# Kernel tuning notes

Measured on AMD Instinct MI355X. Metric: run time of the kernel, lower is better.

## Reference

```python
import jax, jax.numpy as jnp
import numpy as np

B, S, D = 2, 2048, 1024
H, DA, DL = 8, 64, 64   # heads, attention_dim, linear_dim
L = 2                    # num_blocks


def _layernorm(x, w, b, eps):
    mu = jnp.mean(x, axis=-1, keepdims=True)
    var = jnp.mean(jnp.square(x - mu), axis=-1, keepdims=True)
    return (x - mu) * jax.lax.rsqrt(var + eps) * w + b


def _norm_no_affine(x, eps):
    mu = jnp.mean(x, axis=-1, keepdims=True)
    var = jnp.mean(jnp.square(x - mu), axis=-1, keepdims=True)
    return (x - mu) * jax.lax.rsqrt(var + eps)


def setup_inputs() -> dict:
    key = jax.random.key(0)
    ks = jax.random.split(key, 8)
    x = jax.random.normal(ks[0], (B, S, D), dtype=jnp.float32)
    # causal visibility mask: True = visible
    attn_mask = jnp.tril(jnp.ones((S, S), dtype=bool))[None].repeat(B, axis=0)
    proj_dim = DL * 2 * H + DA * 2 * H  # 2048
    uvqk = jax.random.normal(ks[1], (L, D, proj_dim), dtype=jnp.float32) * 0.02
    o_w = jax.random.normal(ks[2], (L, D, DL * H), dtype=jnp.float32) * 0.02  # torch [out,in]
    o_b = jnp.zeros((L, D), dtype=jnp.float32)
    ln_w = jnp.ones((L, D), dtype=jnp.float32)
    ln_b = jnp.zeros((L, D), dtype=jnp.float32)
    last_ln_w = jnp.ones((D,), dtype=jnp.float32)
    last_ln_b = jnp.zeros((D,), dtype=jnp.float32)
    return {"x": x, "attn_mask": attn_mask, "uvqk": uvqk, "o_w": o_w,
            "o_b": o_b, "ln_w": ln_w, "ln_b": ln_b,
            "last_ln_w": last_ln_w, "last_ln_b": last_ln_b}


def reference(x, attn_mask, uvqk, o_w, o_b, ln_w, ln_b, last_ln_w, last_ln_b):
    seq_len = x.shape[1]
    m = attn_mask[:, None, :, :]  # [B,1,S,S]
    for i in range(L):
        h = _layernorm(x, ln_w[i], ln_b[i], 1e-6)                 # [B,S,D]
        proj = jax.nn.silu(jnp.einsum('bsd,de->bse', h, uvqk[i]))  # [B,S,2*(DL+DA)*H]
        u, v, q, k = jnp.split(proj, [DL * H, 2 * DL * H, 2 * DL * H + DA * H], axis=-1)
        q = q.reshape(B, seq_len, H, DA).transpose(0, 2, 1, 3)   # [B,H,S,DA]
        kk = k.reshape(B, seq_len, H, DA).transpose(0, 2, 1, 3)
        vv = v.reshape(B, seq_len, H, DL).transpose(0, 2, 1, 3)  # [B,H,S,DL]
        uu = u.reshape(B, seq_len, H, DL).transpose(0, 2, 1, 3)
        scores = jnp.einsum('bhsd,bhtd->bhst', q, kk)            # [B,H,S,S]
        scores = jnp.where(m, jax.nn.silu(scores) / seq_len, 0.0)
        out = jnp.einsum('bhst,bhtd->bhsd', scores, vv)          # [B,H,S,DL]
        out = _norm_no_affine(out, 1e-6)
        u_dot = (uu * out).transpose(0, 2, 1, 3).reshape(B, seq_len, DL * H)
        x = x + jnp.einsum('bsf,df->bsd', u_dot, o_w[i]) + o_b[i]
    return _layernorm(x, last_ln_w, last_ln_b, 1e-8)
```

## Files before the change

### kernel.cpp

```cpp
#include <hip/hip_runtime.h>

#define B_ 2
#define S_ 2048
#define D_ 1024
#define H_ 8
#define L_ 2
#define P_ 2048
#define F_ 512
#define R_ (B_*S_)

typedef unsigned short u16;
typedef unsigned int u32;
typedef __bf16 bf16;
typedef bf16 bf16x8 __attribute__((ext_vector_type(8)));
typedef short short8 __attribute__((ext_vector_type(8)));
typedef float v4f __attribute__((ext_vector_type(4)));

__device__ __forceinline__ float silu_fast(float x){
  float e = __expf(-x);
  return x * __builtin_amdgcn_rcpf(1.0f + e);
}
__device__ __forceinline__ float bf2f(u16 u){
  union { u32 i; float f; } x; x.i = ((u32)u) << 16; return x.f;
}
__device__ __forceinline__ u16 f2bfu(float f){
  union { float f; u32 i; } x; x.f = f;
  u32 r = x.i + 0x7fff + ((x.i >> 16) & 1);
  return (u16)(r >> 16);
}
__device__ __forceinline__ u16 f2bft(float f){
  union { float f; u32 i; } x; x.f = f;
  return (u16)(x.i >> 16);
}
__device__ __forceinline__ void gload16(const u16* g, u16* l){
  __builtin_amdgcn_global_load_lds(
      (const __attribute__((address_space(1))) void*)g,
      (__attribute__((address_space(3))) void*)l, 16, 0, 0);
}

__global__ __launch_bounds__(256) void cvt_bf16_kernel(const float* __restrict__ src, u16* __restrict__ dst){
  int i = (blockIdx.x * 256 + threadIdx.x) * 4;
  float4 v = *(const float4*)(src + i);
  ushort4 o; o.x = f2bfu(v.x); o.y = f2bfu(v.y); o.z = f2bfu(v.z); o.w = f2bfu(v.w);
  *(ushort4*)(dst + i) = o;
}

__global__ __launch_bounds__(256) void cvt_uvqkT_kernel(const float* __restrict__ uvqk, u16* __restrict__ ot){
  __shared__ float t[32][33];
  int l = blockIdx.z;
  int p0 = blockIdx.x * 32, d0 = blockIdx.y * 32;
  int tx = threadIdx.x & 31, ty = threadIdx.x >> 5;
  const float* src = uvqk + ((size_t)l * D_ + d0) * P_ + p0;
  #pragma unroll
  for (int s = 0; s < 4; s++)
    t[ty + s*8][tx] = src[(size_t)(ty + s*8) * P_ + tx];
  __syncthreads();
  u16* dst = ot + ((size_t)l * P_ + p0) * D_ + d0;
  #pragma unroll
  for (int s = 0; s < 4; s++)
    dst[(size_t)(ty + s*8) * D_ + tx] = f2bfu(t[tx][ty + s*8]);
}

__global__ __launch_bounds__(256) void kvpack_kernel(const u16* __restrict__ projh,
    u16* __restrict__ kpack, u16* __restrict__ vpack){
  __shared__ u16 tls[64*72];
  int t = blockIdx.x, t0 = t * 64;
  int bh = blockIdx.y;
  int b = bh >> 3, hh = bh & 7;
  int tid = threadIdx.x;
  const size_t bS = (size_t)b * S_;
  const int voff = F_ + hh*64, koff = 3*F_ + hh*64;
  {
    int row = tid >> 2, c16 = (tid & 3) * 16;
    const u16* sp = projh + (bS + t0 + row) * P_ + voff + c16;
    short8 a = *(const short8*)sp;
    short8 bq = *(const short8*)(sp + 8);
    *(short8*)&tls[row*72 + c16] = a;
    *(short8*)&tls[row*72 + c16 + 8] = bq;
  }
  __syncthreads();
  size_t obase = ((size_t)(bh*32 + t) * 8) * 512;
  #pragma unroll
  for (int pass = 0; pass < 2; pass++){
    int id = tid + pass * 256;
    int c = id >> 6, lane = id & 63;
    int quad = lane >> 4, l15 = lane & 15;
    int cns = c >> 1, ckst = c & 1;
    const u16* kp = projh + (bS + t0 + cns*16 + l15) * P_ + koff + ckst*32 + quad*8;
    *(short8*)(kpack + obase + (size_t)c*512 + lane*8) = *(const short8*)kp;
    short8 vv;
    #pragma unroll
    for (int j = 0; j < 8; j++)
      vv[j] = (short)tls[(ckst*32 + quad*8 + j)*72 + cns*16 + l15];
    *(short8*)(vpack + obase + (size_t)c*512 + lane*8) = vv;
  }
}

__global__ __launch_bounds__(256) void ln_kernel(const float* __restrict__ src,
    const float* __restrict__ w, const float* __restrict__ b,
    void* __restrict__ outp, float eps, int out_bf16){
  int row = blockIdx.x, tid = threadIdx.x;
  const float* xr = src + (size_t)row * D_;
  float4 v = *(const float4*)(xr + tid * 4);
  float s  = v.x + v.y + v.z + v.w;
  float sq = v.x*v.x + v.y*v.y + v.z*v.z + v.w*v.w;
  #pragma unroll
  for (int off = 32; off; off >>= 1){ s += __shfl_down(s, off); sq += __shfl_down(sq, off); }
  __shared__ float red[8];
  __shared__ float stats[2];
  int wid = tid >> 6;
  if ((tid & 63) == 0){ red[wid] = s; red[4 + wid] = sq; }
  __syncthreads();
  if (tid == 0){
    float S1 = red[0] + red[1] + red[2] + red[3];
    float S2 = red[4] + red[5] + red[6] + red[7];
    float mu = S1 * (1.0f / D_);
    float var = S2 * (1.0f / D_) - mu * mu;
    stats[0] = mu; stats[1] = rsqrtf(var + eps);
  }
  __syncthreads();
  float mu = stats[0], rs = stats[1];
  int i = tid * 4;
  float4 wv = *(const float4*)(w + i);
  float4 bv = *(const float4*)(b + i);
  float o0 = (v.x - mu) * rs * wv.x + bv.x;
  float o1 = (v.y - mu) * rs * wv.y + bv.y;
  float o2 = (v.z - mu) * rs * wv.z + bv.z;
  float o3 = (v.w - mu) * rs * wv.w + bv.w;
  if (out_bf16){
    ushort4 o; o.x = f2bfu(o0); o.y = f2bfu(o1); o.z = f2bfu(o2); o.w = f2bfu(o3);
    *(ushort4*)((u16*)outp + (size_t)row * D_ + i) = o;
  } else {
    *(float4*)((float*)outp + (size_t)row * D_ + i) = make_float4(o0, o1, o2, o3);
  }
}

template<int KDIM, int BKC>
__device__ __forceinline__ void gemm_mfma_core(const u16* __restrict__ A,
    const u16* __restrict__ Bt, u16* As, u16* Bs, int m0, int n0, v4f acc[4][4]){
  int tid = threadIdx.x;
  int w = tid >> 6, lane = tid & 63;
  int wm = w >> 1, wn = w & 1, quad = lane >> 4, l15 = lane & 15;
  int srow = lane >> 2, skoct = (lane & 3) * 8;
  for (int kt = 0; kt < KDIM; kt += BKC*32){
    __syncthreads();
    #pragma unroll
    for (int s = 0; s < 2; s++){
      int g = w * 2 + s;
      #pragma unroll
      for (int kc = 0; kc < BKC; kc++){
        gload16(A  + (size_t)(m0 + g*16 + srow) * KDIM + kt + kc*32 + skoct,
                As + (g*BKC + kc)*512);
        gload16(Bt + (size_t)(n0 + g*16 + srow) * KDIM + kt + kc*32 + skoct,
                Bs + (g*BKC + kc)*512);
      }
    }
    __syncthreads();
    #pragma unroll
    for (int kc = 0; kc < BKC; kc++){
      short8 af[4], bfr[4];
      #pragma unroll
      for (int i = 0; i < 4; i++)
        af[i] = *(const short8*)&As[((wm*4 + i)*BKC + kc)*512 + l15*32 + quad*8];
      #pragma unroll
      for (int j = 0; j < 4; j++)
        bfr[j] = *(const short8*)&Bs[((wn*4 + j)*BKC + kc)*512 + l15*32 + quad*8];
      #pragma unroll
      for (int i = 0; i < 4; i++)
        #pragma unroll
        for (int j = 0; j < 4; j++)
          acc[i][j] = __builtin_amdgcn_mfma_f32_16x16x32_bf16(
              __builtin_bit_cast(bf16x8, af[i]), __builtin_bit_cast(bf16x8, bfr[j]),
              acc[i][j], 0, 0, 0);
    }
  }
}

__global__ __launch_bounds__(256) void gemm_silu_mfma(const u16* __restrict__ A,
    const u16* __restrict__ Bt, u16* __restrict__ C){
  __shared__ u16 As[128*128], Bs[128*128];
  v4f acc[4][4];
  #pragma unroll
  for (int i = 0; i < 4; i++)
    #pragma unroll
    for (int j = 0; j < 4; j++) acc[i][j] = (v4f){0.f,0.f,0.f,0.f};
  int f = blockIdx.x;
  int wg = (f & 7) * 64 + (f >> 3);
  int bx = wg & 15, by = wg >> 4;
  int m0 = by * 128, n0 = bx * 128;
  gemm_mfma_core<D_, 4>(A, Bt, As, Bs, m0, n0, acc);
  int tid = threadIdx.x, w = tid >> 6, lane = tid & 63;
  int wm = w >> 1, wn = w & 1, quad = lane >> 4, l15 = lane & 15;
  #pragma unroll
  for (int i = 0; i < 4; i++)
    #pragma unroll
    for (int r = 0; r < 4; r++){
      int m = m0 + wm*64 + i*16 + quad*4 + r;
      u16* cp = C + (size_t)m * P_ + n0 + wn*64 + l15;
      #pragma unroll
      for (int j = 0; j < 4; j++)
        cp[j*16] = f2bfu(silu_fast(acc[i][j][r]));
    }
}

__global__ __launch_bounds__(256) void gemm_add_mfma(const u16* __restrict__ A,
    const u16* __restrict__ Bt, const float* __restrict__ bias,
    const float* __restrict__ Xin, float* __restrict__ Xout){
  __shared__ u16 As[128*256], Bs[128*256];
  v4f acc[4][4];
  #pragma unroll
  for (int i = 0; i < 4; i++)
    #pragma unroll
    for (int j = 0; j < 4; j++) acc[i][j] = (v4f){0.f,0.f,0.f,0.f};
  int f = blockIdx.x;
  int wg = (f & 7) * 32 + (f >> 3);
  int bx = wg & 7, by = wg >> 3;
  int m0 = by * 128, n0 = bx * 128;
  gemm_mfma_core<F_, 8>(A, Bt, As, Bs, m0, n0, acc);
  int tid = threadIdx.x, w = tid >> 6, lane = tid & 63;
  int wm = w >> 1, wn = w & 1, quad = lane >> 4, l15 = lane & 15;
  float bj[4];
  #pragma unroll
  for (int j = 0; j < 4; j++) bj[j] = bias[n0 + wn*64 + j*16 + l15];
  #pragma unroll
  for (int i = 0; i < 4; i++)
    #pragma unroll
    for (int r = 0; r < 4; r++){
      int m = m0 + wm*64 + i*16 + quad*4 + r;
      size_t off = (size_t)m * D_ + n0 + wn*64 + l15;
      const float* xi = Xin + off;
      float* xo = Xout + off;
      #pragma unroll
      for (int j = 0; j < 4; j++)
        xo[j*16] = xi[j*16] + acc[i][j][r] + bj[j];
    }
}

__global__ __launch_bounds__(256) void attn_kernel(const u16* __restrict__ projh,
                                                   const u16* __restrict__ kpack,
                                                   const u16* __restrict__ vpack,
                                                   u16* __restrict__ udot){
  __shared__ u16 Ps[64*72];
  int f = (int)blockIdx.x;
  int g = f & 7;
  int s = f >> 3;
  int c = s & 31;
  int slot = s >> 5;
  int hx = c >> 4;
  int x = c & 15;
  int qt = slot ? x : (15 - x);
  int bh = g + (slot << 3);
  int dtile = 2*qt + hx;
  int b = bh >> 3, hh = bh & 7;
  int tid = threadIdx.x;
  int w = tid >> 6, lane = tid & 63, quad = lane >> 4, l15 = lane & 15;
  int s0 = qt * 128 + hx * 64;
  const size_t bS = (size_t)b * S_;
  const int qoff = 2*F_ + hh*64;

  bf16x8 aq[2];
  {
    const u16* qp = projh + (bS + s0 + w*16 + l15) * P_ + qoff + quad*8;
    aq[0] = __builtin_bit_cast(bf16x8, *(const short8*)qp);
    aq[1] = __builtin_bit_cast(bf16x8, *(const short8*)(qp + 32));
  }

  v4f oacc[4];
  #pragma unroll
  for (int i = 0; i < 4; i++) oacc[i] = (v4f){0.f, 0.f, 0.f, 0.f};

  auto LOADT = [&](short8 (&BK)[4][2], short8 (&VF)[4][2], int tt){
    size_t pb = ((size_t)(bh*32 + tt) * 8) * 512;
    #pragma unroll
    for (int cc = 0; cc < 8; cc++){
      BK[cc>>1][cc&1] = *(const short8*)(kpack + pb + (size_t)cc*512 + lane*8);
      VF[cc>>1][cc&1] = *(const short8*)(vpack + pb + (size_t)cc*512 + lane*8);
    }
  };

  auto COMPUTE = [&](const short8 (&BK)[4][2], const short8 (&VF)[4][2], int t){
    v4f sacc[4];
    #pragma unroll
    for (int i = 0; i < 4; i++) sacc[i] = (v4f){0.f, 0.f, 0.f, 0.f};
    #pragma unroll
    for (int ns = 0; ns < 4; ns++){
      sacc[ns] = __builtin_amdgcn_mfma_f32_16x16x32_bf16(aq[0],
          __builtin_bit_cast(bf16x8, BK[ns][0]), sacc[ns], 0, 0, 0);
      sacc[ns] = __builtin_amdgcn_mfma_f32_16x16x32_bf16(aq[1],
          __builtin_bit_cast(bf16x8, BK[ns][1]), sacc[ns], 0, 0, 0);
    }
    bool diag = (t == dtile);
    #pragma unroll
    for (int ns = 0; ns < 4; ns++){
      #pragma unroll
      for (int r = 0; r < 4; r++){
        int rl = w*16 + quad*4 + r;
        int cl = ns*16 + l15;
        float p = silu_fast(sacc[ns][r]) * (1.0f / S_);
        if (diag && cl > rl) p = 0.0f;
        Ps[rl*72 + cl] = f2bft(p);
      }
    }
    #pragma unroll
    for (int kst = 0; kst < 2; kst++){
      short8 aps = *(const short8*)&Ps[(w*16 + l15)*72 + kst*32 + quad*8];
      bf16x8 ap = __builtin_bit_cast(bf16x8, aps);
      #pragma unroll
      for (int ds = 0; ds < 4; ds++)
        oacc[ds] = __builtin_amdgcn_mfma_f32_16x16x32_bf16(
            ap, __builtin_bit_cast(bf16x8, VF[ds][kst]), oacc[ds], 0, 0, 0);
    }
  };

  short8 kA[4][2], vA[4][2], kB[4][2], vB[4][2];
  int t = 0;
  LOADT(kA, vA, 0);
  for (;;){
    if (t + 1 <= dtile){
      LOADT(kB, vB, t + 1);
      COMPUTE(kA, vA, t);
      t++;
    } else {
      COMPUTE(kA, vA, t);
      break;
    }
    if (t + 1 <= dtile){
      LOADT(kA, vA, t + 1);
      COMPUTE(kB, vB, t);
      t++;
    } else {
      COMPUTE(kB, vB, t);
      break;
    }
  }

  #pragma unroll
  for (int r = 0; r < 4; r++){
    int sg = s0 + w*16 + quad*4 + r;
    float e0 = oacc[0][r], e1 = oacc[1][r], e2 = oacc[2][r], e3 = oacc[3][r];
    float sm = e0 + e1 + e2 + e3;
    float sq = e0*e0 + e1*e1 + e2*e2 + e3*e3;
    #pragma unroll
    for (int m = 1; m < 16; m <<= 1){
      sm += __shfl_xor(sm, m, 64);
      sq += __shfl_xor(sq, m, 64);
    }
    float mu = sm * (1.0f/64.0f);
    float var = sq * (1.0f/64.0f) - mu*mu;
    float rs = rsqrtf(var + 1e-6f);
    const u16* up = projh + (bS + sg) * P_ + hh*64 + l15;
    u16* dp = udot + (bS + sg) * (size_t)F_ + hh*64 + l15;
    float e[4] = {e0, e1, e2, e3};
    #pragma unroll
    for (int ds = 0; ds < 4; ds++)
      dp[ds*16] = f2bfu((e[ds] - mu) * rs * bf2f(up[ds*16]));
  }
}

extern "C" void kernel_launch(void* const* d_in, const int* in_sizes, int n_in,
                              void* d_out, int out_size, void* d_ws, size_t ws_size,
                              hipStream_t stream){
  (void)in_sizes; (void)n_in; (void)out_size; (void)ws_size;
  const float* x     = (const float*)d_in[0];
  const float* uvqk  = (const float*)d_in[2];
  const float* o_w   = (const float*)d_in[3];
  const float* o_b   = (const float*)d_in[4];
  const float* ln_w  = (const float*)d_in[5];
  const float* ln_b  = (const float*)d_in[6];
  const float* lln_w = (const float*)d_in[7];
  const float* lln_b = (const float*)d_in[8];
  float* out = (float*)d_out;

  char* ws = (char*)d_ws;
  float* xf    = (float*)ws;
  u16*   h     = (u16*)(ws + (16u<<20));
  u16*   kpack = h;
  u16*   vpack = (u16*)(ws + (20u<<20));
  u16*   udot  = (u16*)(ws + (24u<<20));
  u16*   projh = (u16*)(ws + (28u<<20));
  u16*   uvqkT = (u16*)(ws + (44u<<20));
  u16*   owh   = (u16*)(ws + (52u<<20));

  cvt_uvqkT_kernel<<<dim3(P_/32, D_/32, L_), 256, 0, stream>>>(uvqk, uvqkT);
  cvt_bf16_kernel<<<L_ * D_ * F_ / 1024, 256, 0, stream>>>(o_w, owh);
  for (int l = 0; l < L_; l++){
    const float* xsrc = (l == 0) ? x : xf;
    ln_kernel<<<R_, 256, 0, stream>>>(xsrc, ln_w + l * D_, ln_b + l * D_, h, 1e-6f, 1);
    gemm_silu_mfma<<<512, 256, 0, stream>>>(
        h, uvqkT + (size_t)l * P_ * D_, projh);
    kvpack_kernel<<<dim3(S_/64, B_*H_), 256, 0, stream>>>(projh, kpack, vpack);
    attn_kernel<<<512, 256, 0, stream>>>(projh, kpack, vpack, udot);
    gemm_add_mfma<<<256, 256, 0, stream>>>(
        udot, owh + (size_t)l * D_ * F_, o_b + l * D_, xsrc, xf);
  }
  ln_kernel<<<R_, 256, 0, stream>>>(xf, lln_w, lln_b, out, 1e-8f, 0);
}
```

Measured before the change: 269.9 us.

## Stage attention K/V tiles through double-buffered LDS with direct global-to-LDS loads

Before this change, each of the four waves loaded the full K/V tile from global memory into its own registers. Now each wave loads a quarter of the tile into a shared LDS double buffer using direct global-to-LDS loads (gload16). The loads are gated by vmcnt waits and block barriers so the prefetch of tile t+2 overlaps compute on tile t. This cuts redundant global traffic four-fold and frees registers. In exchange it adds two barriers per tile, LDS reads, and 32KB of extra shared memory that may reduce occupancy.

Measured after the change: 290.9 us. +7.8%, slower.

```diff
diff --git a/kernel.cpp b/kernel.cpp
--- a/kernel.cpp
+++ b/kernel.cpp
@@ -240,6 +240,8 @@
                                                    const u16* __restrict__ kpack,
                                                    const u16* __restrict__ vpack,
                                                    u16* __restrict__ udot){
+  __shared__ u16 ks[2][8*512];
+  __shared__ u16 vs[2][8*512];
   __shared__ u16 Ps[64*72];
   int f = (int)blockIdx.x;
   int g = f & 7;
@@ -269,25 +271,32 @@
   #pragma unroll
   for (int i = 0; i < 4; i++) oacc[i] = (v4f){0.f, 0.f, 0.f, 0.f};
 
-  auto LOADT = [&](short8 (&BK)[4][2], short8 (&VF)[4][2], int tt){
+  auto STAGE = [&](int buf, int tt){
     size_t pb = ((size_t)(bh*32 + tt) * 8) * 512;
     #pragma unroll
-    for (int cc = 0; cc < 8; cc++){
-      BK[cc>>1][cc&1] = *(const short8*)(kpack + pb + (size_t)cc*512 + lane*8);
-      VF[cc>>1][cc&1] = *(const short8*)(vpack + pb + (size_t)cc*512 + lane*8);
+    for (int cc = 0; cc < 2; cc++){
+      int ch = w*2 + cc;
+      gload16(kpack + pb + (size_t)ch*512 + lane*8, &ks[buf][ch*512]);
+      gload16(vpack + pb + (size_t)ch*512 + lane*8, &vs[buf][ch*512]);
     }
   };
 
-  auto COMPUTE = [&](const short8 (&BK)[4][2], const short8 (&VF)[4][2], int t){
+  auto COMPUTE = [&](int buf, int t){
+    short8 vf[4][2];
+    #pragma unroll
+    for (int ds = 0; ds < 4; ds++)
+      #pragma unroll
+      for (int kst = 0; kst < 2; kst++)
+        vf[ds][kst] = *(const short8*)&vs[buf][(ds*2+kst)*512 + lane*8];
     v4f sacc[4];
     #pragma unroll
     for (int i = 0; i < 4; i++) sacc[i] = (v4f){0.f, 0.f, 0.f, 0.f};
     #pragma unroll
     for (int ns = 0; ns < 4; ns++){
-      sacc[ns] = __builtin_amdgcn_mfma_f32_16x16x32_bf16(aq[0],
-          __builtin_bit_cast(bf16x8, BK[ns][0]), sacc[ns], 0, 0, 0);
-      sacc[ns] = __builtin_amdgcn_mfma_f32_16x16x32_bf16(aq[1],
-          __builtin_bit_cast(bf16x8, BK[ns][1]), sacc[ns], 0, 0, 0);
+      bf16x8 bk0 = __builtin_bit_cast(bf16x8, *(const short8*)&ks[buf][(ns*2+0)*512 + lane*8]);
+      bf16x8 bk1 = __builtin_bit_cast(bf16x8, *(const short8*)&ks[buf][(ns*2+1)*512 + lane*8]);
+      sacc[ns] = __builtin_amdgcn_mfma_f32_16x16x32_bf16(aq[0], bk0, sacc[ns], 0, 0, 0);
+      sacc[ns] = __builtin_amdgcn_mfma_f32_16x16x32_bf16(aq[1], bk1, sacc[ns], 0, 0, 0);
     }
     bool diag = (t == dtile);
     #pragma unroll
@@ -308,30 +317,34 @@
       #pragma unroll
       for (int ds = 0; ds < 4; ds++)
         oacc[ds] = __builtin_amdgcn_mfma_f32_16x16x32_bf16(
-            ap, __builtin_bit_cast(bf16x8, VF[ds][kst]), oacc[ds], 0, 0, 0);
+            ap, __builtin_bit_cast(bf16x8, vf[ds][kst]), oacc[ds], 0, 0, 0);
     }
   };
 
-  short8 kA[4][2], vA[4][2], kB[4][2], vB[4][2];
-  int t = 0;
-  LOADT(kA, vA, 0);
-  for (;;){
-    if (t + 1 <= dtile){
-      LOADT(kB, vB, t + 1);
-      COMPUTE(kA, vA, t);
-      t++;
+  STAGE(0, 0);
+  if (dtile >= 1){
+    STAGE(1, 1);
+    asm volatile("s_waitcnt vmcnt(4)" ::: "memory");
+  } else {
+    asm volatile("s_waitcnt vmcnt(0)" ::: "memory");
+  }
+  __builtin_amdgcn_s_barrier();
+  int cur = 0;
+  for (int t = 0; ; ){
+    COMPUTE(cur, t);
+    if (t == dtile) break;
+    __builtin_amdgcn_sched_barrier(0);
+    __builtin_amdgcn_s_barrier();
+    if (t + 2 <= dtile){
+      STAGE(cur, t + 2);
+      asm volatile("s_waitcnt vmcnt(4)" ::: "memory");
     } else {
-      COMPUTE(kA, vA, t);
-      break;
-    }
-    if (t + 1 <= dtile){
-      LOADT(kA, vA, t + 1);
-      COMPUTE(kB, vB, t);
-      t++;
-    } else {
-      COMPUTE(kB, vB, t);
-      break;
-    }
+      asm volatile("s_waitcnt vmcnt(0)" ::: "memory");
+    }
+    __builtin_amdgcn_sched_barrier(0);
+    __builtin_amdgcn_s_barrier();
+    cur ^= 1;
+    t++;
   }
 
   #pragma unroll
```
